# Optimization experiments

Hardware: AMD Instinct MI355X
Metric: run time of the kernel (lower is better)

Reference implementation:

```python
import jax, jax.numpy as jnp
import numpy as np

IN_CH, C_M, C_N = 512, 512, 128
B, H, W = 16, 56, 56


def setup_inputs() -> dict:
    key = jax.random.key(0)
    ks = jax.random.split(key, 7)
    s = 1.0 / np.sqrt(IN_CH)
    return {
        "x": jax.random.normal(ks[0], (B, IN_CH, H, W), dtype=jnp.float32),
        "wA": jax.random.uniform(ks[1], (C_M, IN_CH), jnp.float32, -s, s),
        "bA": jax.random.uniform(ks[2], (C_M,), jnp.float32, -s, s),
        "wB": jax.random.uniform(ks[3], (C_N, IN_CH), jnp.float32, -s, s),
        "bB": jax.random.uniform(ks[4], (C_N,), jnp.float32, -s, s),
        "wV": jax.random.uniform(ks[5], (C_N, IN_CH), jnp.float32, -s, s),
        "bV": jax.random.uniform(ks[6], (C_N,), jnp.float32, -s, s),
        "K": 1,
    }


def reference(x, wA, bA, wB, bB, wV, bV, K):
    b, c, h, w = x.shape
    c_m, c_n = wA.shape[0], wB.shape[0]
    batch = b // K
    hw = h * w
    N = K * hw
    # 1x1 convs == channel-wise matmuls
    A = jnp.einsum('bchw,mc->bmhw', x, wA) + bA[None, :, None, None]
    Bf = jnp.einsum('bchw,nc->bnhw', x, wB) + bB[None, :, None, None]
    Vf = jnp.einsum('bchw,nc->bnhw', x, wV) + bV[None, :, None, None]
    # (batch, c_m, K*h*w)
    tmpA = A.reshape(batch, K, c_m, hw).transpose(0, 2, 1, 3).reshape(batch, c_m, N)
    # softmax over the spatial dim N (torch Softmax() on 2D -> dim=1)
    tmpB = Bf.reshape(batch, K, c_n, hw).transpose(0, 2, 1, 3).reshape(batch, c_n, N)
    attB = jax.nn.softmax(tmpB, axis=-1).transpose(0, 2, 1)  # (batch, N, c_n)
    # softmax over channel dim c_n
    tmpV = Vf.reshape(batch, K, c_n, hw).transpose(0, 1, 3, 2).reshape(batch, N, c_n)
    attV = jax.nn.softmax(tmpV, axis=-1).transpose(0, 2, 1)  # (batch, c_n, N)
    G = jnp.matmul(tmpA, attB)   # (batch, c_m, c_n) global descriptors
    Z = jnp.matmul(G, attV)      # (batch, c_m, N) distribute
    Z = Z.reshape(batch, c_m, K, hw).transpose(0, 2, 1, 3).reshape(b, c_m, h, w)
    return Z
```

## Files before the change

kernel.cpp:

```cpp
#include <hip/hip_runtime.h>
#include <hip/hip_bf16.h>

#define BATCH 16
#define CIN   512
#define HW    3136
#define CM    512
#define CN    128
#define CBV   256

typedef short short8 __attribute__((ext_vector_type(8)));
typedef float f32x4  __attribute__((ext_vector_type(4)));

#define MFMA(a,b,c) __builtin_amdgcn_mfma_f32_16x16x32_bf16((a),(b),(c),0,0,0)

__device__ __forceinline__ void cvt_store8(__bf16* dst, const float* src) {
  const f32x4 a = *(const f32x4*)src;
  const f32x4 b = *(const f32x4*)(src + 4);
  __attribute__((aligned(16))) __bf16 t[8];
  t[0] = (__bf16)a[0]; t[1] = (__bf16)a[1]; t[2] = (__bf16)a[2]; t[3] = (__bf16)a[3];
  t[4] = (__bf16)b[0]; t[5] = (__bf16)b[1]; t[6] = (__bf16)b[2]; t[7] = (__bf16)b[3];
  *(uint4*)dst = *(uint4*)t;
}

__global__ __launch_bounds__(256) void wcast_kernel(
    const float* __restrict__ wB, const float* __restrict__ wV,
    const float* __restrict__ wA, __bf16* __restrict__ Wbf)
{
  size_t i = (size_t)blockIdx.x*2048 + (size_t)threadIdx.x*8;
  const float* src; size_t off;
  if (i < 65536)       { src = wB; off = i; }
  else if (i < 131072) { src = wV; off = i - 65536; }
  else                 { src = wA; off = i - 131072; }
  cvt_store8(Wbf + i, src + off);
}

__global__ __launch_bounds__(256) void transpose_x_kernel(
    const float* __restrict__ x, __bf16* __restrict__ xT)
{
  const int s0 = blockIdx.x * 64;
  const int c0 = blockIdx.y * 128;
  const int b  = blockIdx.z;
  const int tid = threadIdx.x;
  __shared__ __attribute__((aligned(16))) __bf16 T[64*136];

  const float* xb = x + ((size_t)b*CIN + c0)*HW + s0;
  const int sg = tid & 15, cr = tid >> 4;
  #pragma unroll
  for (int p = 0; p < 8; ++p) {
    int c = cr + 16*p;
    f32x4 v = *(const f32x4*)(xb + (size_t)c*HW + sg*4);
    #pragma unroll
    for (int j = 0; j < 4; ++j) T[(sg*4 + j)*136 + c] = (__bf16)v[j];
  }
  __syncthreads();
  __bf16* dst = xT + ((size_t)b*HW + s0)*CIN + c0;
  const int cg = tid & 15, sr = tid >> 4;
  #pragma unroll
  for (int p = 0; p < 4; ++p) {
    int srow = sr + 16*p;
    *(uint4*)&dst[(size_t)srow*CIN + cg*8] = *(uint4*)&T[srow*136 + cg*8];
  }
}

__global__ __launch_bounds__(256) void conv_bv_kernel(
    const __bf16* __restrict__ Wbf, const __bf16* __restrict__ xT,
    const float* __restrict__ bB, const float* __restrict__ bV,
    __bf16* __restrict__ BV)
{
  const int s0  = blockIdx.x * 64;
  const int b   = blockIdx.y;
  const int tid = threadIdx.x;
  const int lane = tid & 63, w = tid >> 6;
  const int l15  = lane & 15, q = lane >> 4;

  __shared__ __attribute__((aligned(16))) __bf16 Wt[256*72];
  __shared__ __attribute__((aligned(16))) __bf16 Xt[64*72];

  f32x4 acc[4][4] = {};
  const __bf16* xTb = xT + (size_t)b*HW*CIN;
  const int colg = tid & 7, row0 = tid >> 3;

  for (int k0 = 0; k0 < CIN; k0 += 64) {
    #pragma unroll
    for (int p = 0; p < 8; ++p) {
      int row = row0 + 32*p;
      *(uint4*)&Wt[row*72 + colg*8] = *(const uint4*)(Wbf + (size_t)row*CIN + k0 + colg*8);
    }
    #pragma unroll
    for (int p = 0; p < 2; ++p) {
      int row = row0 + 32*p;
      *(uint4*)&Xt[row*72 + colg*8] = *(const uint4*)(xTb + (size_t)(s0+row)*CIN + k0 + colg*8);
    }
    __syncthreads();
    #pragma unroll
    for (int kk = 0; kk < 2; ++kk) {
      short8 a[4], bb[4];
      #pragma unroll
      for (int mi = 0; mi < 4; ++mi)
        a[mi] = *(short8*)&Wt[(w*64 + mi*16 + l15)*72 + kk*32 + q*8];
      #pragma unroll
      for (int si = 0; si < 4; ++si)
        bb[si] = *(short8*)&Xt[(si*16 + l15)*72 + kk*32 + q*8];
      #pragma unroll
      for (int mi = 0; mi < 4; ++mi)
        #pragma unroll
        for (int si = 0; si < 4; ++si)
          acc[mi][si] = MFMA(a[mi], bb[si], acc[mi][si]);
    }
    __syncthreads();
  }

  const size_t outb = (size_t)b * CBV * HW;
  #pragma unroll
  for (int mi = 0; mi < 4; ++mi)
    #pragma unroll
    for (int si = 0; si < 4; ++si) {
      int s = s0 + si*16 + l15;
      #pragma unroll
      for (int r = 0; r < 4; ++r) {
        int nch = w*64 + mi*16 + q*4 + r;
        float bias = (nch < CN) ? bB[nch] : bV[nch-CN];
        BV[outb + (size_t)nch*HW + s] = (__bf16)(acc[mi][si][r] + bias);
      }
    }
}

__global__ __launch_bounds__(256) void conv_bv_gather_kernel(
    const float* __restrict__ x,
    const float* __restrict__ wB, const float* __restrict__ bB,
    const float* __restrict__ wV, const float* __restrict__ bV,
    __bf16* __restrict__ BV)
{
  const int s0  = blockIdx.x * 64;
  const int b   = blockIdx.y;
  const int tid = threadIdx.x;
  const int lane = tid & 63, w = tid >> 6;
  const int l15  = lane & 15, q = lane >> 4;

  __shared__ __attribute__((aligned(16))) __bf16 Wt[256*72];
  __shared__ __attribute__((aligned(16))) __bf16 Xt[64*72];

  f32x4 acc[4][4] = {};
  const float* xb = x + (size_t)b * CIN * HW;
  const int colg = tid & 7, row0 = tid >> 3;
  const int s_l = tid & 63, cb = tid >> 6;

  for (int k0 = 0; k0 < CIN; k0 += 64) {
    #pragma unroll
    for (int p = 0; p < 8; ++p) {
      int row = row0 + 32*p;
      const float* src = (row < 128) ? (wB + row*512) : (wV + (row-128)*512);
      cvt_store8(&Wt[row*72 + colg*8], src + k0 + colg*8);
    }
    #pragma unroll
    for (int p = 0; p < 2; ++p) {
      int cg = cb + 4*p;
      __attribute__((aligned(16))) __bf16 tmp[8];
      #pragma unroll
      for (int j = 0; j < 8; ++j)
        tmp[j] = (__bf16)xb[(size_t)(k0 + cg*8 + j)*HW + s0 + s_l];
      *(uint4*)&Xt[s_l*72 + cg*8] = *(uint4*)tmp;
    }
    __syncthreads();
    #pragma unroll
    for (int kk = 0; kk < 2; ++kk) {
      short8 a[4], bb[4];
      #pragma unroll
      for (int mi = 0; mi < 4; ++mi)
        a[mi] = *(short8*)&Wt[(w*64 + mi*16 + l15)*72 + kk*32 + q*8];
      #pragma unroll
      for (int si = 0; si < 4; ++si)
        bb[si] = *(short8*)&Xt[(si*16 + l15)*72 + kk*32 + q*8];
      #pragma unroll
      for (int mi = 0; mi < 4; ++mi)
        #pragma unroll
        for (int si = 0; si < 4; ++si)
          acc[mi][si] = MFMA(a[mi], bb[si], acc[mi][si]);
    }
    __syncthreads();
  }

  const size_t outb = (size_t)b * CBV * HW;
  #pragma unroll
  for (int mi = 0; mi < 4; ++mi)
    #pragma unroll
    for (int si = 0; si < 4; ++si) {
      int s = s0 + si*16 + l15;
      #pragma unroll
      for (int r = 0; r < 4; ++r) {
        int nch = w*64 + mi*16 + q*4 + r;
        float bias = (nch < CN) ? bB[nch] : bV[nch-CN];
        BV[outb + (size_t)nch*HW + s] = (__bf16)(acc[mi][si][r] + bias);
      }
    }
}

__global__ __launch_bounds__(256) void softmax_b_kernel(__bf16* __restrict__ BV)
{
  const int n = blockIdx.x, b = blockIdx.y;
  __bf16* row = BV + ((size_t)b*CBV + n)*HW;
  const int tid = threadIdx.x;

  float v[13];
  float mx = -1e30f;
  #pragma unroll
  for (int i = 0; i < 13; ++i) {
    int idx = tid + i*256;
    v[i] = (idx < HW) ? (float)row[idx] : -1e30f;
    mx = fmaxf(mx, v[i]);
  }
  #pragma unroll
  for (int off = 32; off > 0; off >>= 1) mx = fmaxf(mx, __shfl_down(mx, off));
  __shared__ float redm[4], reds[4];
  if ((tid & 63) == 0) redm[tid >> 6] = mx;
  __syncthreads();
  float m = fmaxf(fmaxf(redm[0], redm[1]), fmaxf(redm[2], redm[3]));

  float sum = 0.f;
  #pragma unroll
  for (int i = 0; i < 13; ++i) { v[i] = __expf(v[i] - m); sum += v[i]; }
  #pragma unroll
  for (int off = 32; off > 0; off >>= 1) sum += __shfl_down(sum, off);
  if ((tid & 63) == 0) reds[tid >> 6] = sum;
  __syncthreads();
  float inv = 1.0f / (reds[0] + reds[1] + reds[2] + reds[3]);

  #pragma unroll
  for (int i = 0; i < 13; ++i) {
    int idx = tid + i*256;
    if (idx < HW) row[idx] = (__bf16)(v[i] * inv);
  }
}

__global__ __launch_bounds__(256) void softmax_v_t_kernel(
    const __bf16* __restrict__ BV, __bf16* __restrict__ attVT)
{
  const int s0 = blockIdx.x * 64, b = blockIdx.y;
  const int tid = threadIdx.x;
  const int s_l = tid & 63, jg = tid >> 6;
  const __bf16* vb = BV + ((size_t)b*CBV + CN)*HW + s0 + s_l;

  float v[32];
  float mx = -1e30f;
  #pragma unroll
  for (int i = 0; i < 32; ++i) {
    v[i] = (float)vb[(size_t)(jg*32 + i)*HW];
    mx = fmaxf(mx, v[i]);
  }
  __shared__ float red[4][64];
  red[jg][s_l] = mx;
  __syncthreads();
  float m = fmaxf(fmaxf(red[0][s_l], red[1][s_l]), fmaxf(red[2][s_l], red[3][s_l]));
  float sum = 0.f;
  #pragma unroll
  for (int i = 0; i < 32; ++i) { v[i] = __expf(v[i] - m); sum += v[i]; }
  __syncthreads();
  red[jg][s_l] = sum;
  __syncthreads();
  float inv = 1.0f / (red[0][s_l] + red[1][s_l] + red[2][s_l] + red[3][s_l]);

  __shared__ __attribute__((aligned(16))) __bf16 T[64*136];
  #pragma unroll
  for (int u = 0; u < 4; ++u) {
    __attribute__((aligned(16))) __bf16 tmp[8];
    #pragma unroll
    for (int j = 0; j < 8; ++j) tmp[j] = (__bf16)(v[u*8 + j] * inv);
    *(uint4*)&T[s_l*136 + jg*32 + u*8] = *(uint4*)tmp;
  }
  __syncthreads();
  __bf16* dst = attVT + ((size_t)b*HW + s0)*CN;
  const int g = tid & 15, r0 = tid >> 4;
  #pragma unroll
  for (int p = 0; p < 4; ++p) {
    int row = r0 + 16*p;
    *(uint4*)&dst[row*CN + g*8] = *(uint4*)&T[row*136 + g*8];
  }
}

__global__ __launch_bounds__(256) void h_gemm_kernel(
    const float* __restrict__ x, const __bf16* __restrict__ attB,
    float* __restrict__ H)
{
  const int c0 = blockIdx.x * 64, b = blockIdx.y, kc = blockIdx.z;
  const int tid = threadIdx.x, lane = tid & 63, w = tid >> 6;
  const int l15 = lane & 15, q = lane >> 4;

  __shared__ __attribute__((aligned(16))) __bf16 At[64*72];
  __shared__ __attribute__((aligned(16))) __bf16 Bt[128*72];
  f32x4 acc[4][2] = {};

  const float* xb = x + ((size_t)b*CIN + c0)*HW;
  const __bf16* ab = attB + (size_t)b*CBV*HW;
  const int colg = tid & 7, row0 = tid >> 3;

  for (int ki = 0; ki < 7; ++ki) {
    int k0 = kc*448 + ki*64;
    #pragma unroll
    for (int p = 0; p < 2; ++p) {
      int row = row0 + 32*p;
      cvt_store8(&At[row*72 + colg*8], xb + (size_t)row*HW + k0 + colg*8);
    }
    #pragma unroll
    for (int p = 0; p < 4; ++p) {
      int row = row0 + 32*p;
      *(uint4*)&Bt[row*72 + colg*8] = *(const uint4*)(ab + (size_t)row*HW + k0 + colg*8);
    }
    __syncthreads();
    #pragma unroll
    for (int kk = 0; kk < 2; ++kk) {
      short8 a[4], bb[2];
      #pragma unroll
      for (int mi = 0; mi < 4; ++mi)
        a[mi] = *(short8*)&At[(mi*16 + l15)*72 + kk*32 + q*8];
      #pragma unroll
      for (int ni = 0; ni < 2; ++ni)
        bb[ni] = *(short8*)&Bt[(w*32 + ni*16 + l15)*72 + kk*32 + q*8];
      #pragma unroll
      for (int mi = 0; mi < 4; ++mi)
        #pragma unroll
        for (int ni = 0; ni < 2; ++ni)
          acc[mi][ni] = MFMA(a[mi], bb[ni], acc[mi][ni]);
    }
    __syncthreads();
  }

  float* Hb = H + (size_t)b*CIN*CN;
  #pragma unroll
  for (int mi = 0; mi < 4; ++mi)
    #pragma unroll
    for (int ni = 0; ni < 2; ++ni)
      #pragma unroll
      for (int r = 0; r < 4; ++r) {
        int c = c0 + mi*16 + q*4 + r;
        int n = w*32 + ni*16 + l15;
        atomicAdd(&Hb[c*CN + n], acc[mi][ni][r]);
      }
}

__global__ __launch_bounds__(256) void g_gemm_kernel(
    const __bf16* __restrict__ wAbf, const float* __restrict__ bA,
    const float* __restrict__ H, __bf16* __restrict__ G)
{
  const int m0 = blockIdx.x * 64, b = blockIdx.y;
  const int tid = threadIdx.x, lane = tid & 63, w = tid >> 6;
  const int l15 = lane & 15, q = lane >> 4;

  __shared__ __attribute__((aligned(16))) __bf16 At[64*72];
  __shared__ __attribute__((aligned(16))) __bf16 Bt[128*72];
  f32x4 acc[4][2] = {};

  const float* Hb = H + (size_t)b*CIN*CN;
  const int colg = tid & 7, row0 = tid >> 3;
  const int nn = tid & 127, gh = tid >> 7;

  for (int k0 = 0; k0 < CIN; k0 += 64) {
    #pragma unroll
    for (int p = 0; p < 2; ++p) {
      int row = row0 + 32*p;
      *(uint4*)&At[row*72 + colg*8] = *(const uint4*)(wAbf + (size_t)(m0+row)*CIN + k0 + colg*8);
    }
    #pragma unroll
    for (int p = 0; p < 4; ++p) {
      int g = gh + 2*p;
      __attribute__((aligned(16))) __bf16 tmp[8];
      #pragma unroll
      for (int j = 0; j < 8; ++j)
        tmp[j] = (__bf16)Hb[(size_t)(k0 + g*8 + j)*CN + nn];
      *(uint4*)&Bt[nn*72 + g*8] = *(uint4*)tmp;
    }
    __syncthreads();
    #pragma unroll
    for (int kk = 0; kk < 2; ++kk) {
      short8 a[4], bb[2];
      #pragma unroll
      for (int mi = 0; mi < 4; ++mi)
        a[mi] = *(short8*)&At[(mi*16 + l15)*72 + kk*32 + q*8];
      #pragma unroll
      for (int ni = 0; ni < 2; ++ni)
        bb[ni] = *(short8*)&Bt[(w*32 + ni*16 + l15)*72 + kk*32 + q*8];
      #pragma unroll
      for (int mi = 0; mi < 4; ++mi)
        #pragma unroll
        for (int ni = 0; ni < 2; ++ni)
          acc[mi][ni] = MFMA(a[mi], bb[ni], acc[mi][ni]);
    }
    __syncthreads();
  }

  #pragma unroll
  for (int mi = 0; mi < 4; ++mi)
    #pragma unroll
    for (int ni = 0; ni < 2; ++ni)
      #pragma unroll
      for (int r = 0; r < 4; ++r) {
        int m = m0 + mi*16 + q*4 + r;
        int n = w*32 + ni*16 + l15;
        G[((size_t)b*CM + m)*CN + n] = (__bf16)(acc[mi][ni][r] + bA[m]);
      }
}

__global__ __launch_bounds__(256) void g_gemm_f32w_kernel(
    const float* __restrict__ wA, const float* __restrict__ bA,
    const float* __restrict__ H, __bf16* __restrict__ G)
{
  const int m0 = blockIdx.x * 64, b = blockIdx.y;
  const int tid = threadIdx.x, lane = tid & 63, w = tid >> 6;
  const int l15 = lane & 15, q = lane >> 4;

  __shared__ __attribute__((aligned(16))) __bf16 At[64*72];
  __shared__ __attribute__((aligned(16))) __bf16 Bt[128*72];
  f32x4 acc[4][2] = {};

  const float* Hb = H + (size_t)b*CIN*CN;
  const int colg = tid & 7, row0 = tid >> 3;
  const int nn = tid & 127, gh = tid >> 7;

  for (int k0 = 0; k0 < CIN; k0 += 64) {
    #pragma unroll
    for (int p = 0; p < 2; ++p) {
      int row = row0 + 32*p;
      cvt_store8(&At[row*72 + colg*8], wA + (size_t)(m0+row)*CIN + k0 + colg*8);
    }
    #pragma unroll
    for (int p = 0; p < 4; ++p) {
      int g = gh + 2*p;
      __attribute__((aligned(16))) __bf16 tmp[8];
      #pragma unroll
      for (int j = 0; j < 8; ++j)
        tmp[j] = (__bf16)Hb[(size_t)(k0 + g*8 + j)*CN + nn];
      *(uint4*)&Bt[nn*72 + g*8] = *(uint4*)tmp;
    }
    __syncthreads();
    #pragma unroll
    for (int kk = 0; kk < 2; ++kk) {
      short8 a[4], bb[2];
      #pragma unroll
      for (int mi = 0; mi < 4; ++mi)
        a[mi] = *(short8*)&At[(mi*16 + l15)*72 + kk*32 + q*8];
      #pragma unroll
      for (int ni = 0; ni < 2; ++ni)
        bb[ni] = *(short8*)&Bt[(w*32 + ni*16 + l15)*72 + kk*32 + q*8];
      #pragma unroll
      for (int mi = 0; mi < 4; ++mi)
        #pragma unroll
        for (int ni = 0; ni < 2; ++ni)
          acc[mi][ni] = MFMA(a[mi], bb[ni], acc[mi][ni]);
    }
    __syncthreads();
  }

  #pragma unroll
  for (int mi = 0; mi < 4; ++mi)
    #pragma unroll
    for (int ni = 0; ni < 2; ++ni)
      #pragma unroll
      for (int r = 0; r < 4; ++r) {
        int m = m0 + mi*16 + q*4 + r;
        int n = w*32 + ni*16 + l15;
        G[((size_t)b*CM + m)*CN + n] = (__bf16)(acc[mi][ni][r] + bA[m]);
      }
}

__global__ __launch_bounds__(256) void z_gemm_kernel(
    const __bf16* __restrict__ G, const __bf16* __restrict__ attVT,
    float* __restrict__ out)
{
  const int m0 = blockIdx.x * 128, s0 = blockIdx.y * 64, b = blockIdx.z;
  const int tid = threadIdx.x, lane = tid & 63, w = tid >> 6;
  const int l15 = lane & 15, q = lane >> 4;

  __shared__ __attribute__((aligned(16))) __bf16 At[128*136];
  __shared__ __attribute__((aligned(16))) __bf16 Bt[64*136];

  const __bf16* Gb = G + ((size_t)b*CM + m0)*CN;
  const __bf16* Vb = attVT + ((size_t)b*HW + s0)*CN;
  const int g = tid & 15, r0 = tid >> 4;
  #pragma unroll
  for (int p = 0; p < 8; ++p) {
    int row = r0 + 16*p;
    *(uint4*)&At[row*136 + g*8] = *(const uint4*)(Gb + (size_t)row*CN + g*8);
  }
  #pragma unroll
  for (int p = 0; p < 4; ++p) {
    int row = r0 + 16*p;
    *(uint4*)&Bt[row*136 + g*8] = *(const uint4*)(Vb + (size_t)row*CN + g*8);
  }
  __syncthreads();

  f32x4 acc[8] = {};
  #pragma unroll
  for (int kk = 0; kk < 4; ++kk) {
    short8 bb = *(short8*)&Bt[(w*16 + l15)*136 + kk*32 + q*8];
    #pragma unroll
    for (int mi = 0; mi < 8; ++mi) {
      short8 a = *(short8*)&At[(mi*16 + l15)*136 + kk*32 + q*8];
      acc[mi] = MFMA(a, bb, acc[mi]);
    }
  }

  const int s = s0 + w*16 + l15;
  #pragma unroll
  for (int mi = 0; mi < 8; ++mi)
    #pragma unroll
    for (int r = 0; r < 4; ++r) {
      int m = m0 + mi*16 + q*4 + r;
      out[((size_t)b*CM + m)*HW + s] = acc[mi][r];
    }
}

extern "C" void kernel_launch(void* const* d_in, const int* in_sizes, int n_in,
                              void* d_out, int out_size, void* d_ws, size_t ws_size,
                              hipStream_t stream)
{
  (void)in_sizes; (void)n_in; (void)out_size;
  const float* x  = (const float*)d_in[0];
  const float* wA = (const float*)d_in[1];
  const float* bA = (const float*)d_in[2];
  const float* wB = (const float*)d_in[3];
  const float* bB = (const float*)d_in[4];
  const float* wV = (const float*)d_in[5];
  const float* bV = (const float*)d_in[6];
  float* out = (float*)d_out;

  char* ws = (char*)d_ws;
  const size_t szXT    = (size_t)BATCH*HW*CIN*2;
  const size_t szWBF   = (size_t)(128*512 + 128*512 + 512*512)*2;
  const size_t szBV    = (size_t)BATCH*CBV*HW*2;
  const size_t szAttVT = (size_t)BATCH*HW*CN*2;
  const size_t szH     = (size_t)BATCH*CIN*CN*4;
  const size_t szG     = (size_t)BATCH*CM*CN*2;
  const size_t needMain = szXT + szWBF + szBV + szAttVT + szH + szG;

  if (ws_size >= needMain) {
    __bf16* xT    = (__bf16*)(ws);
    __bf16* Wbf   = (__bf16*)(ws + szXT);
    __bf16* BV    = (__bf16*)(ws + szXT + szWBF);
    __bf16* attVT = (__bf16*)(ws + szXT + szWBF + szBV);
    float*  H     = (float*) (ws + szXT + szWBF + szBV + szAttVT);
    __bf16* G     = (__bf16*)(ws + szXT + szWBF + szBV + szAttVT + szH);
    __bf16* wAbf  = Wbf + 2*128*512;

    wcast_kernel      <<<dim3(192),     256, 0, stream>>>(wB, wV, wA, Wbf);
    transpose_x_kernel<<<dim3(49,4,16), 256, 0, stream>>>(x, xT);
    conv_bv_kernel    <<<dim3(49,16),   256, 0, stream>>>(Wbf, xT, bB, bV, BV);
    softmax_b_kernel  <<<dim3(128,16),  256, 0, stream>>>(BV);
    softmax_v_t_kernel<<<dim3(49,16),   256, 0, stream>>>(BV, attVT);
    hipMemsetAsync(H, 0, szH, stream);
    h_gemm_kernel     <<<dim3(8,16,7),  256, 0, stream>>>(x, BV, H);
    g_gemm_kernel     <<<dim3(8,16),    256, 0, stream>>>(wAbf, bA, H, G);
    z_gemm_kernel     <<<dim3(4,49,16), 256, 0, stream>>>(G, attVT, out);
  } else {
    __bf16* BV    = (__bf16*)(ws);
    __bf16* attVT = (__bf16*)(ws + szBV);
    float*  H     = (float*) (ws + szBV + szAttVT);
    __bf16* G     = (__bf16*)(ws + szBV + szAttVT + szH);

    conv_bv_gather_kernel<<<dim3(49,16),   256, 0, stream>>>(x, wB, bB, wV, bV, BV);
    softmax_b_kernel     <<<dim3(128,16),  256, 0, stream>>>(BV);
    softmax_v_t_kernel   <<<dim3(49,16),   256, 0, stream>>>(BV, attVT);
    hipMemsetAsync(H, 0, szH, stream);
    h_gemm_kernel        <<<dim3(8,16,7),  256, 0, stream>>>(x, BV, H);
    g_gemm_f32w_kernel   <<<dim3(8,16),    256, 0, stream>>>(wA, bA, H, G);
    z_gemm_kernel        <<<dim3(4,49,16), 256, 0, stream>>>(G, attVT, out);
  }
}
```

Baseline: 311.4 us.

## Fuse V softmax into conv epilogue, emit bf16 x copy, fold B softmax into H GEMM

The transpose kernel now also writes a bf16 copy of x in channel-major layout, so the H GEMM reads bf16 instead of fp32 x. The conv kernel computes the channel softmax for V directly in its epilogue and writes the transposed attVT tile, which removes the separate softmax_v_t pass and the V half of the BV buffer. The B softmax is split into a small stats kernel (row max and inverse sum) and an on-the-fly exp/normalise inside the H GEMM tile loader, which removes a read-modify-write pass over B. In exchange it adds an extra bf16 x buffer and its write traffic, recomputes exp inside the GEMM loader, and uses larger H GEMM tiles with fewer blocks.

```diff
diff --git a/kernel.cpp b/kernel.cpp
--- a/kernel.cpp
+++ b/kernel.cpp
@@ -35,7 +35,7 @@
 }
 
 __global__ __launch_bounds__(256) void transpose_x_kernel(
-    const float* __restrict__ x, __bf16* __restrict__ xT)
+    const float* __restrict__ x, __bf16* __restrict__ xT, __bf16* __restrict__ xbf)
 {
   const int s0 = blockIdx.x * 64;
   const int c0 = blockIdx.y * 128;
@@ -43,14 +43,21 @@
   const int tid = threadIdx.x;
   __shared__ __attribute__((aligned(16))) __bf16 T[64*136];
 
-  const float* xb = x + ((size_t)b*CIN + c0)*HW + s0;
-  const int sg = tid & 15, cr = tid >> 4;
-  #pragma unroll
-  for (int p = 0; p < 8; ++p) {
-    int c = cr + 16*p;
-    f32x4 v = *(const f32x4*)(xb + (size_t)c*HW + sg*4);
-    #pragma unroll
-    for (int j = 0; j < 4; ++j) T[(sg*4 + j)*136 + c] = (__bf16)v[j];
+  const float* xsrc = x + ((size_t)b*CIN + c0)*HW + s0;
+  __bf16* xdst      = xbf + ((size_t)b*CIN + c0)*HW + s0;
+  const int colg = tid & 7, row0 = tid >> 3;
+  #pragma unroll
+  for (int p = 0; p < 4; ++p) {
+    int c = row0 + 32*p;
+    const float* sp = xsrc + (size_t)c*HW + colg*8;
+    f32x4 v0 = *(const f32x4*)sp;
+    f32x4 v1 = *(const f32x4*)(sp + 4);
+    __attribute__((aligned(16))) __bf16 t[8];
+    t[0]=(__bf16)v0[0]; t[1]=(__bf16)v0[1]; t[2]=(__bf16)v0[2]; t[3]=(__bf16)v0[3];
+    t[4]=(__bf16)v1[0]; t[5]=(__bf16)v1[1]; t[6]=(__bf16)v1[2]; t[7]=(__bf16)v1[3];
+    *(uint4*)(xdst + (size_t)c*HW + colg*8) = *(uint4*)t;
+    #pragma unroll
+    for (int j = 0; j < 8; ++j) T[(colg*8 + j)*136 + c] = t[j];
   }
   __syncthreads();
   __bf16* dst = xT + ((size_t)b*HW + s0)*CIN + c0;
@@ -65,7 +72,7 @@
 __global__ __launch_bounds__(256) void conv_bv_kernel(
     const __bf16* __restrict__ Wbf, const __bf16* __restrict__ xT,
     const float* __restrict__ bB, const float* __restrict__ bV,
-    __bf16* __restrict__ BV)
+    __bf16* __restrict__ BVB, __bf16* __restrict__ attVT)
 {
   const int s0  = blockIdx.x * 64;
   const int b   = blockIdx.y;
@@ -73,8 +80,12 @@
   const int lane = tid & 63, w = tid >> 6;
   const int l15  = lane & 15, q = lane >> 4;
 
-  __shared__ __attribute__((aligned(16))) __bf16 Wt[256*72];
-  __shared__ __attribute__((aligned(16))) __bf16 Xt[64*72];
+  __shared__ __attribute__((aligned(16))) char smem[46080];
+  __bf16* Wt = (__bf16*)smem;
+  __bf16* Xt = (__bf16*)(smem + 36864);
+  __bf16* T  = (__bf16*)smem;
+  __shared__ float Vm[2][64];
+  __shared__ float Vs[2][64];
 
   f32x4 acc[4][4] = {};
   const __bf16* xTb = xT + (size_t)b*HW*CIN;
@@ -90,6 +101,364 @@
     for (int p = 0; p < 2; ++p) {
       int row = row0 + 32*p;
       *(uint4*)&Xt[row*72 + colg*8] = *(const uint4*)(xTb + (size_t)(s0+row)*CIN + k0 + colg*8);
+    }
+    __syncthreads();
+    #pragma unroll
+    for (int kk = 0; kk < 2; ++kk) {
+      short8 a[4], bb[4];
+      #pragma unroll
+      for (int mi = 0; mi < 4; ++mi)
+        a[mi] = *(short8*)&Wt[(w*64 + mi*16 + l15)*72 + kk*32 + q*8];
+      #pragma unroll
+      for (int si = 0; si < 4; ++si)
+        bb[si] = *(short8*)&Xt[(si*16 + l15)*72 + kk*32 + q*8];
+      #pragma unroll
+      for (int mi = 0; mi < 4; ++mi)
+        #pragma unroll
+        for (int si = 0; si < 4; ++si)
+          acc[mi][si] = MFMA(a[mi], bb[si], acc[mi][si]);
+    }
+    __syncthreads();
+  }
+
+  float bias[4][4];
+  #pragma unroll
+  for (int mi = 0; mi < 4; ++mi)
+    #pragma unroll
+    for (int r = 0; r < 4; ++r) {
+      int nch = w*64 + mi*16 + q*4 + r;
+      bias[mi][r] = (nch < CN) ? bB[nch] : bV[nch - CN];
+    }
+
+  if (w < 2) {
+    const size_t outb = (size_t)b * CN * HW;
+    #pragma unroll
+    for (int mi = 0; mi < 4; ++mi)
+      #pragma unroll
+      for (int si = 0; si < 4; ++si) {
+        int s = s0 + si*16 + l15;
+        #pragma unroll
+        for (int r = 0; r < 4; ++r) {
+          int nch = w*64 + mi*16 + q*4 + r;
+          BVB[outb + (size_t)nch*HW + s] = (__bf16)(acc[mi][si][r] + bias[mi][r]);
+        }
+      }
+  } else {
+    #pragma unroll
+    for (int si = 0; si < 4; ++si) {
+      float m = -1e30f;
+      #pragma unroll
+      for (int mi = 0; mi < 4; ++mi)
+        #pragma unroll
+        for (int r = 0; r < 4; ++r)
+          m = fmaxf(m, acc[mi][si][r] + bias[mi][r]);
+      m = fmaxf(m, __shfl_xor(m, 16));
+      m = fmaxf(m, __shfl_xor(m, 32));
+      if (q == 0) Vm[w-2][si*16 + l15] = m;
+    }
+  }
+  __syncthreads();
+  if (w >= 2) {
+    #pragma unroll
+    for (int si = 0; si < 4; ++si) {
+      int idx = si*16 + l15;
+      float ms = fmaxf(Vm[0][idx], Vm[1][idx]);
+      float ssum = 0.f;
+      #pragma unroll
+      for (int mi = 0; mi < 4; ++mi)
+        #pragma unroll
+        for (int r = 0; r < 4; ++r) {
+          float e = __expf(acc[mi][si][r] + bias[mi][r] - ms);
+          acc[mi][si][r] = e;
+          ssum += e;
+        }
+      ssum += __shfl_xor(ssum, 16);
+      ssum += __shfl_xor(ssum, 32);
+      if (q == 0) Vs[w-2][idx] = ssum;
+    }
+  }
+  __syncthreads();
+  if (w >= 2) {
+    #pragma unroll
+    for (int si = 0; si < 4; ++si) {
+      int idx = si*16 + l15;
+      float inv = 1.0f / (Vs[0][idx] + Vs[1][idx]);
+      #pragma unroll
+      for (int mi = 0; mi < 4; ++mi)
+        #pragma unroll
+        for (int r = 0; r < 4; ++r) {
+          int j = (w-2)*64 + mi*16 + q*4 + r;
+          T[idx*136 + j] = (__bf16)(acc[mi][si][r] * inv);
+        }
+    }
+  }
+  __syncthreads();
+  __bf16* dst = attVT + ((size_t)b*HW + s0)*CN;
+  #pragma unroll
+  for (int k = 0; k < 4; ++k) {
+    int chunk = tid + 256*k;
+    int row = chunk >> 4, oct = chunk & 15;
+    *(uint4*)&dst[(size_t)row*CN + oct*8] = *(uint4*)&T[row*136 + oct*8];
+  }
+}
+
+__global__ __launch_bounds__(256) void bstats_kernel(
+    const __bf16* __restrict__ BVB, float* __restrict__ sm, float* __restrict__ sinv)
+{
+  const int row = blockIdx.x*4 + (threadIdx.x >> 6);
+  const int lane = threadIdx.x & 63;
+  const __bf16* rp = BVB + (size_t)row*HW;
+
+  uint4 raw[7];
+  float mx = -1e30f;
+  #pragma unroll
+  for (int i = 0; i < 6; ++i) {
+    raw[i] = *(const uint4*)(rp + (lane + 64*i)*8);
+    const __bf16* v = (const __bf16*)&raw[i];
+    #pragma unroll
+    for (int j = 0; j < 8; ++j) mx = fmaxf(mx, (float)v[j]);
+  }
+  if (lane < 8) {
+    raw[6] = *(const uint4*)(rp + (lane + 384)*8);
+    const __bf16* v = (const __bf16*)&raw[6];
+    #pragma unroll
+    for (int j = 0; j < 8; ++j) mx = fmaxf(mx, (float)v[j]);
+  }
+  #pragma unroll
+  for (int off = 1; off < 64; off <<= 1) mx = fmaxf(mx, __shfl_xor(mx, off));
+
+  float sum = 0.f;
+  #pragma unroll
+  for (int i = 0; i < 6; ++i) {
+    const __bf16* v = (const __bf16*)&raw[i];
+    #pragma unroll
+    for (int j = 0; j < 8; ++j) sum += __expf((float)v[j] - mx);
+  }
+  if (lane < 8) {
+    const __bf16* v = (const __bf16*)&raw[6];
+    #pragma unroll
+    for (int j = 0; j < 8; ++j) sum += __expf((float)v[j] - mx);
+  }
+  #pragma unroll
+  for (int off = 1; off < 64; off <<= 1) sum += __shfl_xor(sum, off);
+
+  if (lane == 0) { sm[row] = mx; sinv[row] = 1.0f / sum; }
+}
+
+__global__ __launch_bounds__(256) void h_gemm_kernel(
+    const __bf16* __restrict__ xbf, const __bf16* __restrict__ BVB,
+    const float* __restrict__ sm, const float* __restrict__ sinv,
+    float* __restrict__ H)
+{
+  const int c0 = blockIdx.x * 128, b = blockIdx.y, kc = blockIdx.z;
+  const int tid = threadIdx.x, lane = tid & 63, w = tid >> 6;
+  const int l15 = lane & 15, q = lane >> 4;
+
+  __shared__ __attribute__((aligned(16))) __bf16 At[128*72];
+  __shared__ __attribute__((aligned(16))) __bf16 Bt[128*72];
+  f32x4 acc[8][2] = {};
+
+  const __bf16* xb = xbf + ((size_t)b*CIN + c0)*HW;
+  const __bf16* ab = BVB + (size_t)b*CN*HW;
+  const float* smb = sm + b*CN;
+  const float* sib = sinv + b*CN;
+  const int colg = tid & 7, row0 = tid >> 3;
+
+  for (int ki = 0; ki < 7; ++ki) {
+    int k0 = kc*448 + ki*64;
+    #pragma unroll
+    for (int p = 0; p < 4; ++p) {
+      int row = row0 + 32*p;
+      *(uint4*)&At[row*72 + colg*8] = *(const uint4*)(xb + (size_t)row*HW + k0 + colg*8);
+    }
+    #pragma unroll
+    for (int p = 0; p < 4; ++p) {
+      int row = row0 + 32*p;
+      uint4 rawv = *(const uint4*)(ab + (size_t)row*HW + k0 + colg*8);
+      const __bf16* v = (const __bf16*)&rawv;
+      float mrow = smb[row], irow = sib[row];
+      __attribute__((aligned(16))) __bf16 t[8];
+      #pragma unroll
+      for (int j = 0; j < 8; ++j)
+        t[j] = (__bf16)(__expf((float)v[j] - mrow) * irow);
+      *(uint4*)&Bt[row*72 + colg*8] = *(uint4*)t;
+    }
+    __syncthreads();
+    #pragma unroll
+    for (int kk = 0; kk < 2; ++kk) {
+      short8 a[8], bb[2];
+      #pragma unroll
+      for (int mi = 0; mi < 8; ++mi)
+        a[mi] = *(short8*)&At[(mi*16 + l15)*72 + kk*32 + q*8];
+      #pragma unroll
+      for (int ni = 0; ni < 2; ++ni)
+        bb[ni] = *(short8*)&Bt[(w*32 + ni*16 + l15)*72 + kk*32 + q*8];
+      #pragma unroll
+      for (int mi = 0; mi < 8; ++mi)
+        #pragma unroll
+        for (int ni = 0; ni < 2; ++ni)
+          acc[mi][ni] = MFMA(a[mi], bb[ni], acc[mi][ni]);
+    }
+    __syncthreads();
+  }
+
+  float* Hb = H + (size_t)b*CIN*CN;
+  #pragma unroll
+  for (int mi = 0; mi < 8; ++mi)
+    #pragma unroll
+    for (int ni = 0; ni < 2; ++ni)
+      #pragma unroll
+      for (int r = 0; r < 4; ++r) {
+        int c = c0 + mi*16 + q*4 + r;
+        int n = w*32 + ni*16 + l15;
+        atomicAdd(&Hb[c*CN + n], acc[mi][ni][r]);
+      }
+}
+
+__global__ __launch_bounds__(256) void g_gemm_kernel(
+    const __bf16* __restrict__ wAbf, const float* __restrict__ bA,
+    const float* __restrict__ H, __bf16* __restrict__ G)
+{
+  const int m0 = blockIdx.x * 64, b = blockIdx.y;
+  const int tid = threadIdx.x, lane = tid & 63, w = tid >> 6;
+  const int l15 = lane & 15, q = lane >> 4;
+
+  __shared__ __attribute__((aligned(16))) __bf16 At[64*72];
+  __shared__ __attribute__((aligned(16))) __bf16 Bt[128*72];
+  f32x4 acc[4][2] = {};
+
+  const float* Hb = H + (size_t)b*CIN*CN;
+  const int colg = tid & 7, row0 = tid >> 3;
+  const int nn = tid & 127, gh = tid >> 7;
+
+  for (int k0 = 0; k0 < CIN; k0 += 64) {
+    #pragma unroll
+    for (int p = 0; p < 2; ++p) {
+      int row = row0 + 32*p;
+      *(uint4*)&At[row*72 + colg*8] = *(const uint4*)(wAbf + (size_t)(m0+row)*CIN + k0 + colg*8);
+    }
+    #pragma unroll
+    for (int p = 0; p < 4; ++p) {
+      int g = gh + 2*p;
+      __attribute__((aligned(16))) __bf16 tmp[8];
+      #pragma unroll
+      for (int j = 0; j < 8; ++j)
+        tmp[j] = (__bf16)Hb[(size_t)(k0 + g*8 + j)*CN + nn];
+      *(uint4*)&Bt[nn*72 + g*8] = *(uint4*)tmp;
+    }
+    __syncthreads();
+    #pragma unroll
+    for (int kk = 0; kk < 2; ++kk) {
+      short8 a[4], bb[2];
+      #pragma unroll
+      for (int mi = 0; mi < 4; ++mi)
+        a[mi] = *(short8*)&At[(mi*16 + l15)*72 + kk*32 + q*8];
+      #pragma unroll
+      for (int ni = 0; ni < 2; ++ni)
+        bb[ni] = *(short8*)&Bt[(w*32 + ni*16 + l15)*72 + kk*32 + q*8];
+      #pragma unroll
+      for (int mi = 0; mi < 4; ++mi)
+        #pragma unroll
+        for (int ni = 0; ni < 2; ++ni)
+          acc[mi][ni] = MFMA(a[mi], bb[ni], acc[mi][ni]);
+    }
+    __syncthreads();
+  }
+
+  #pragma unroll
+  for (int mi = 0; mi < 4; ++mi)
+    #pragma unroll
+    for (int ni = 0; ni < 2; ++ni)
+      #pragma unroll
+      for (int r = 0; r < 4; ++r) {
+        int m = m0 + mi*16 + q*4 + r;
+        int n = w*32 + ni*16 + l15;
+        G[((size_t)b*CM + m)*CN + n] = (__bf16)(acc[mi][ni][r] + bA[m]);
+      }
+}
+
+__global__ __launch_bounds__(256) void z_gemm_kernel(
+    const __bf16* __restrict__ G, const __bf16* __restrict__ attVT,
+    float* __restrict__ out)
+{
+  const int m0 = blockIdx.x * 128, s0 = blockIdx.y * 64, b = blockIdx.z;
+  const int tid = threadIdx.x, lane = tid & 63, w = tid >> 6;
+  const int l15 = lane & 15, q = lane >> 4;
+
+  __shared__ __attribute__((aligned(16))) __bf16 At[128*136];
+  __shared__ __attribute__((aligned(16))) __bf16 Bt[64*136];
+
+  const __bf16* Gb = G + ((size_t)b*CM + m0)*CN;
+  const __bf16* Vb = attVT + ((size_t)b*HW + s0)*CN;
+  const int g = tid & 15, r0 = tid >> 4;
+  #pragma unroll
+  for (int p = 0; p < 8; ++p) {
+    int row = r0 + 16*p;
+    *(uint4*)&At[row*136 + g*8] = *(const uint4*)(Gb + (size_t)row*CN + g*8);
+  }
+  #pragma unroll
+  for (int p = 0; p < 4; ++p) {
+    int row = r0 + 16*p;
+    *(uint4*)&Bt[row*136 + g*8] = *(const uint4*)(Vb + (size_t)row*CN + g*8);
+  }
+  __syncthreads();
+
+  f32x4 acc[8] = {};
+  #pragma unroll
+  for (int kk = 0; kk < 4; ++kk) {
+    short8 bb = *(short8*)&Bt[(w*16 + l15)*136 + kk*32 + q*8];
+    #pragma unroll
+    for (int mi = 0; mi < 8; ++mi) {
+      short8 a = *(short8*)&At[(mi*16 + l15)*136 + kk*32 + q*8];
+      acc[mi] = MFMA(a, bb, acc[mi]);
+    }
+  }
+
+  const int s = s0 + w*16 + l15;
+  #pragma unroll
+  for (int mi = 0; mi < 8; ++mi)
+    #pragma unroll
+    for (int r = 0; r < 4; ++r) {
+      int m = m0 + mi*16 + q*4 + r;
+      out[((size_t)b*CM + m)*HW + s] = acc[mi][r];
+    }
+}
+
+__global__ __launch_bounds__(256) void conv_bv_gather_kernel(
+    const float* __restrict__ x,
+    const float* __restrict__ wB, const float* __restrict__ bB,
+    const float* __restrict__ wV, const float* __restrict__ bV,
+    __bf16* __restrict__ BV)
+{
+  const int s0  = blockIdx.x * 64;
+  const int b   = blockIdx.y;
+  const int tid = threadIdx.x;
+  const int lane = tid & 63, w = tid >> 6;
+  const int l15  = lane & 15, q = lane >> 4;
+
+  __shared__ __attribute__((aligned(16))) __bf16 Wt[256*72];
+  __shared__ __attribute__((aligned(16))) __bf16 Xt[64*72];
+
+  f32x4 acc[4][4] = {};
+  const float* xb = x + (size_t)b * CIN * HW;
+  const int colg = tid & 7, row0 = tid >> 3;
+  const int s_l = tid & 63, cb = tid >> 6;
+
+  for (int k0 = 0; k0 < CIN; k0 += 64) {
+    #pragma unroll
+    for (int p = 0; p < 8; ++p) {
+      int row = row0 + 32*p;
+      const float* src = (row < 128) ? (wB + row*512) : (wV + (row-128)*512);
+      cvt_store8(&Wt[row*72 + colg*8], src + k0 + colg*8);
+    }
+    #pragma unroll
+    for (int p = 0; p < 2; ++p) {
+      int cg = cb + 4*p;
+      __attribute__((aligned(16))) __bf16 tmp[8];
+      #pragma unroll
+      for (int j = 0; j < 8; ++j)
+        tmp[j] = (__bf16)xb[(size_t)(k0 + cg*8 + j)*HW + s0 + s_l];
+      *(uint4*)&Xt[s_l*72 + cg*8] = *(uint4*)tmp;
     }
     __syncthreads();
     #pragma unroll
@@ -125,76 +494,6 @@
     }
 }
 
-__global__ __launch_bounds__(256) void conv_bv_gather_kernel(
-    const float* __restrict__ x,
-    const float* __restrict__ wB, const float* __restrict__ bB,
-    const float* __restrict__ wV, const float* __restrict__ bV,
-    __bf16* __restrict__ BV)
-{
-  const int s0  = blockIdx.x * 64;
-  const int b   = blockIdx.y;
-  const int tid = threadIdx.x;
-  const int lane = tid & 63, w = tid >> 6;
-  const int l15  = lane & 15, q = lane >> 4;
-
-  __shared__ __attribute__((aligned(16))) __bf16 Wt[256*72];
-  __shared__ __attribute__((aligned(16))) __bf16 Xt[64*72];
-
-  f32x4 acc[4][4] = {};
-  const float* xb = x + (size_t)b * CIN * HW;
-  const int colg = tid & 7, row0 = tid >> 3;
-  const int s_l = tid & 63, cb = tid >> 6;
-
-  for (int k0 = 0; k0 < CIN; k0 += 64) {
-    #pragma unroll
-    for (int p = 0; p < 8; ++p) {
-      int row = row0 + 32*p;
-      const float* src = (row < 128) ? (wB + row*512) : (wV + (row-128)*512);
-      cvt_store8(&Wt[row*72 + colg*8], src + k0 + colg*8);
-    }
-    #pragma unroll
-    for (int p = 0; p < 2; ++p) {
-      int cg = cb + 4*p;
-      __attribute__((aligned(16))) __bf16 tmp[8];
-      #pragma unroll
-      for (int j = 0; j < 8; ++j)
-        tmp[j] = (__bf16)xb[(size_t)(k0 + cg*8 + j)*HW + s0 + s_l];
-      *(uint4*)&Xt[s_l*72 + cg*8] = *(uint4*)tmp;
-    }
-    __syncthreads();
-    #pragma unroll
-    for (int kk = 0; kk < 2; ++kk) {
-      short8 a[4], bb[4];
-      #pragma unroll
-      for (int mi = 0; mi < 4; ++mi)
-        a[mi] = *(short8*)&Wt[(w*64 + mi*16 + l15)*72 + kk*32 + q*8];
-      #pragma unroll
-      for (int si = 0; si < 4; ++si)
-        bb[si] = *(short8*)&Xt[(si*16 + l15)*72 + kk*32 + q*8];
-      #pragma unroll
-      for (int mi = 0; mi < 4; ++mi)
-        #pragma unroll
-        for (int si = 0; si < 4; ++si)
-          acc[mi][si] = MFMA(a[mi], bb[si], acc[mi][si]);
-    }
-    __syncthreads();
-  }
-
-  const size_t outb = (size_t)b * CBV * HW;
-  #pragma unroll
-  for (int mi = 0; mi < 4; ++mi)
-    #pragma unroll
-    for (int si = 0; si < 4; ++si) {
-      int s = s0 + si*16 + l15;
-      #pragma unroll
-      for (int r = 0; r < 4; ++r) {
-        int nch = w*64 + mi*16 + q*4 + r;
-        float bias = (nch < CN) ? bB[nch] : bV[nch-CN];
-        BV[outb + (size_t)nch*HW + s] = (__bf16)(acc[mi][si][r] + bias);
-      }
-    }
-}
-
 __global__ __launch_bounds__(256) void softmax_b_kernel(__bf16* __restrict__ BV)
 {
   const int n = blockIdx.x, b = blockIdx.y;
@@ -277,7 +576,7 @@
   }
 }
 
-__global__ __launch_bounds__(256) void h_gemm_kernel(
+__global__ __launch_bounds__(256) void h_gemm_f32_kernel(
     const float* __restrict__ x, const __bf16* __restrict__ attB,
     float* __restrict__ H)
 {
@@ -337,8 +636,8 @@
       }
 }
 
-__global__ __launch_bounds__(256) void g_gemm_kernel(
-    const __bf16* __restrict__ wAbf, const float* __restrict__ bA,
+__global__ __launch_bounds__(256) void g_gemm_f32w_kernel(
+    const float* __restrict__ wA, const float* __restrict__ bA,
     const float* __restrict__ H, __bf16* __restrict__ G)
 {
   const int m0 = blockIdx.x * 64, b = blockIdx.y;
@@ -357,7 +656,7 @@
     #pragma unroll
     for (int p = 0; p < 2; ++p) {
       int row = row0 + 32*p;
-      *(uint4*)&At[row*72 + colg*8] = *(const uint4*)(wAbf + (size_t)(m0+row)*CIN + k0 + colg*8);
+      cvt_store8(&At[row*72 + colg*8], wA + (size_t)(m0+row)*CIN + k0 + colg*8);
     }
     #pragma unroll
     for (int p = 0; p < 4; ++p) {
@@ -397,115 +696,6 @@
         int n = w*32 + ni*16 + l15;
         G[((size_t)b*CM + m)*CN + n] = (__bf16)(acc[mi][ni][r] + bA[m]);
       }
-}
-
-__global__ __launch_bounds__(256) void g_gemm_f32w_kernel(
-    const float* __restrict__ wA, const float* __restrict__ bA,
-    const float* __restrict__ H, __bf16* __restrict__ G)
-{
-  const int m0 = blockIdx.x * 64, b = blockIdx.y;
-  const int tid = threadIdx.x, lane = tid & 63, w = tid >> 6;
-  const int l15 = lane & 15, q = lane >> 4;
-
-  __shared__ __attribute__((aligned(16))) __bf16 At[64*72];
-  __shared__ __attribute__((aligned(16))) __bf16 Bt[128*72];
-  f32x4 acc[4][2] = {};
-
-  const float* Hb = H + (size_t)b*CIN*CN;
-  const int colg = tid & 7, row0 = tid >> 3;
-  const int nn = tid & 127, gh = tid >> 7;
-
-  for (int k0 = 0; k0 < CIN; k0 += 64) {
-    #pragma unroll
-    for (int p = 0; p < 2; ++p) {
-      int row = row0 + 32*p;
-      cvt_store8(&At[row*72 + colg*8], wA + (size_t)(m0+row)*CIN + k0 + colg*8);
-    }
-    #pragma unroll
-    for (int p = 0; p < 4; ++p) {
-      int g = gh + 2*p;
-      __attribute__((aligned(16))) __bf16 tmp[8];
-      #pragma unroll
-      for (int j = 0; j < 8; ++j)
-        tmp[j] = (__bf16)Hb[(size_t)(k0 + g*8 + j)*CN + nn];
-      *(uint4*)&Bt[nn*72 + g*8] = *(uint4*)tmp;
-    }
-    __syncthreads();
-    #pragma unroll
-    for (int kk = 0; kk < 2; ++kk) {
-      short8 a[4], bb[2];
-      #pragma unroll
-      for (int mi = 0; mi < 4; ++mi)
-        a[mi] = *(short8*)&At[(mi*16 + l15)*72 + kk*32 + q*8];
-      #pragma unroll
-      for (int ni = 0; ni < 2; ++ni)
-        bb[ni] = *(short8*)&Bt[(w*32 + ni*16 + l15)*72 + kk*32 + q*8];
-      #pragma unroll
-      for (int mi = 0; mi < 4; ++mi)
-        #pragma unroll
-        for (int ni = 0; ni < 2; ++ni)
-          acc[mi][ni] = MFMA(a[mi], bb[ni], acc[mi][ni]);
-    }
-    __syncthreads();
-  }
-
-  #pragma unroll
-  for (int mi = 0; mi < 4; ++mi)
-    #pragma unroll
-    for (int ni = 0; ni < 2; ++ni)
-      #pragma unroll
-      for (int r = 0; r < 4; ++r) {
-        int m = m0 + mi*16 + q*4 + r;
-        int n = w*32 + ni*16 + l15;
-        G[((size_t)b*CM + m)*CN + n] = (__bf16)(acc[mi][ni][r] + bA[m]);
-      }
-}
-
-__global__ __launch_bounds__(256) void z_gemm_kernel(
-    const __bf16* __restrict__ G, const __bf16* __restrict__ attVT,
-    float* __restrict__ out)
-{
-  const int m0 = blockIdx.x * 128, s0 = blockIdx.y * 64, b = blockIdx.z;
-  const int tid = threadIdx.x, lane = tid & 63, w = tid >> 6;
-  const int l15 = lane & 15, q = lane >> 4;
-
-  __shared__ __attribute__((aligned(16))) __bf16 At[128*136];
-  __shared__ __attribute__((aligned(16))) __bf16 Bt[64*136];
-
-  const __bf16* Gb = G + ((size_t)b*CM + m0)*CN;
-  const __bf16* Vb = attVT + ((size_t)b*HW + s0)*CN;
-  const int g = tid & 15, r0 = tid >> 4;
-  #pragma unroll
-  for (int p = 0; p < 8; ++p) {
-    int row = r0 + 16*p;
-    *(uint4*)&At[row*136 + g*8] = *(const uint4*)(Gb + (size_t)row*CN + g*8);
-  }
-  #pragma unroll
-  for (int p = 0; p < 4; ++p) {
-    int row = r0 + 16*p;
-    *(uint4*)&Bt[row*136 + g*8] = *(const uint4*)(Vb + (size_t)row*CN + g*8);
-  }
-  __syncthreads();
-
-  f32x4 acc[8] = {};
-  #pragma unroll
-  for (int kk = 0; kk < 4; ++kk) {
-    short8 bb = *(short8*)&Bt[(w*16 + l15)*136 + kk*32 + q*8];
-    #pragma unroll
-    for (int mi = 0; mi < 8; ++mi) {
-      short8 a = *(short8*)&At[(mi*16 + l15)*136 + kk*32 + q*8];
-      acc[mi] = MFMA(a, bb, acc[mi]);
-    }
-  }
-
-  const int s = s0 + w*16 + l15;
-  #pragma unroll
-  for (int mi = 0; mi < 8; ++mi)
-    #pragma unroll
-    for (int r = 0; r < 4; ++r) {
-      int m = m0 + mi*16 + q*4 + r;
-      out[((size_t)b*CM + m)*HW + s] = acc[mi][r];
-    }
 }
 
 extern "C" void kernel_launch(void* const* d_in, const int* in_sizes, int n_in,
@@ -524,32 +714,38 @@
 
   char* ws = (char*)d_ws;
   const size_t szXT    = (size_t)BATCH*HW*CIN*2;
+  const size_t szXBF   = (size_t)BATCH*CIN*HW*2;
   const size_t szWBF   = (size_t)(128*512 + 128*512 + 512*512)*2;
-  const size_t szBV    = (size_t)BATCH*CBV*HW*2;
+  const size_t szBVB   = (size_t)BATCH*CN*HW*2;
   const size_t szAttVT = (size_t)BATCH*HW*CN*2;
   const size_t szH     = (size_t)BATCH*CIN*CN*4;
   const size_t szG     = (size_t)BATCH*CM*CN*2;
-  const size_t needMain = szXT + szWBF + szBV + szAttVT + szH + szG;
+  const size_t szStats = (size_t)BATCH*CN*4*2;
+  const size_t needMain = szXT + szXBF + szWBF + szBVB + szAttVT + szH + szG + szStats;
 
   if (ws_size >= needMain) {
-    __bf16* xT    = (__bf16*)(ws);
-    __bf16* Wbf   = (__bf16*)(ws + szXT);
-    __bf16* BV    = (__bf16*)(ws + szXT + szWBF);
-    __bf16* attVT = (__bf16*)(ws + szXT + szWBF + szBV);
-    float*  H     = (float*) (ws + szXT + szWBF + szBV + szAttVT);
-    __bf16* G     = (__bf16*)(ws + szXT + szWBF + szBV + szAttVT + szH);
+    char* p = ws;
+    __bf16* xT    = (__bf16*)p; p += szXT;
+    __bf16* xbf   = (__bf16*)p; p += szXBF;
+    __bf16* Wbf   = (__bf16*)p; p += szWBF;
+    __bf16* BVB   = (__bf16*)p; p += szBVB;
+    __bf16* attVT = (__bf16*)p; p += szAttVT;
+    float*  H     = (float*)p;  p += szH;
+    __bf16* G     = (__bf16*)p; p += szG;
+    float*  sm    = (float*)p;  p += (size_t)BATCH*CN*4;
+    float*  sinv  = (float*)p;
     __bf16* wAbf  = Wbf + 2*128*512;
 
     wcast_kernel      <<<dim3(192),     256, 0, stream>>>(wB, wV, wA, Wbf);
-    transpose_x_kernel<<<dim3(49,4,16), 256, 0, stream>>>(x, xT);
-    conv_bv_kernel    <<<dim3(49,16),   256, 0, stream>>>(Wbf, xT, bB, bV, BV);
-    softmax_b_kernel  <<<dim3(128,16),  256, 0, stream>>>(BV);
-    softmax_v_t_kernel<<<dim3(49,16),   256, 0, stream>>>(BV, attVT);
+    transpose_x_kernel<<<dim3(49,4,16), 256, 0, stream>>>(x, xT, xbf);
+    conv_bv_kernel    <<<dim3(49,16),   256, 0, stream>>>(Wbf, xT, bB, bV, BVB, attVT);
+    bstats_kernel     <<<dim3(512),     256, 0, stream>>>(BVB, sm, sinv);
     hipMemsetAsync(H, 0, szH, stream);
-    h_gemm_kernel     <<<dim3(8,16,7),  256, 0, stream>>>(x, BV, H);
+    h_gemm_kernel     <<<dim3(4,16,7),  256, 0, stream>>>(xbf, BVB, sm, sinv, H);
     g_gemm_kernel     <<<dim3(8,16),    256, 0, stream>>>(wAbf, bA, H, G);
     z_gemm_kernel     <<<dim3(4,49,16), 256, 0, stream>>>(G, attVT, out);
   } else {
+    const size_t szBV = (size_t)BATCH*CBV*HW*2;
     __bf16* BV    = (__bf16*)(ws);
     __bf16* attVT = (__bf16*)(ws + szBV);
     float*  H     = (float*) (ws + szBV + szAttVT);
@@ -559,7 +755,7 @@
     softmax_b_kernel     <<<dim3(128,16),  256, 0, stream>>>(BV);
     softmax_v_t_kernel   <<<dim3(49,16),   256, 0, stream>>>(BV, attVT);
     hipMemsetAsync(H, 0, szH, stream);
-    h_gemm_kernel        <<<dim3(8,16,7),  256, 0, stream>>>(x, BV, H);
+    h_gemm_f32_kernel    <<<dim3(8,16,7),  256, 0, stream>>>(x, BV, H);
     g_gemm_f32w_kernel   <<<dim3(8,16),    256, 0, stream>>>(wA, bA, H, G);
     z_gemm_kernel        <<<dim3(4,49,16), 256, 0, stream>>>(G, attVT, out);
   }
```

New measurement: 311.5 us. About the same (+0.0%).
